# Kernel tuning notes

Measured on AMD Instinct MI355X. Metric: run time of the kernel, lower is better.

## Reference

```python
import jax, jax.numpy as jnp
import numpy as np
from jax import lax

# Module constants (from init_kwargs)
K = 1.0            # conductivity
H = 1.0 / 1023.0   # grid spacing
VALUE = 0.0        # Dirichlet boundary value
STENCIL = np.array([[0.0, 0.25, 0.0],
                    [0.25, 0.0, 0.25],
                    [0.0, 0.25, 0.0]], dtype=np.float32)


def setup_inputs() -> dict:
    key = jax.random.key(0)
    k1, k2 = jax.random.split(key)
    B, C, Hn, Wn = 16, 1, 1024, 1024
    u = jax.random.normal(k1, (B, C, Hn, Wn), dtype=jnp.float32)
    f = jax.random.normal(k2, (B, C, Hn, Wn), dtype=jnp.float32)
    # conv weight: (out=1, in=1, 3, 3), repeated over in_channels (=1 here)
    weight = jnp.asarray(STENCIL).reshape(1, 1, 3, 3)
    return {"u": u, "f": f, "weight": weight}


def reference(u, f, weight):
    # v = detached interior of u, padded with the Dirichlet value
    v_int = lax.stop_gradient(u[..., 1:-1, 1:-1])           # [B,1,H-2,W-2]
    v = jnp.pad(v_int, ((0, 0), (0, 0), (1, 1), (1, 1)),
                mode="constant", constant_values=VALUE)      # [B,1,H,W]
    # 5-point Jacobi stencil, VALID conv -> interior shape [B,1,H-2,W-2]
    conv = lax.conv_general_dilated(
        v, weight, window_strides=(1, 1), padding="VALID",
        dimension_numbers=("NCHW", "OIHW", "NCHW"))
    cof = -(H ** 2) / (K * 4.0)
    source = lax.stop_gradient((cof * f)[..., 1:-1, 1:-1])
    # interior <- stencil(v) + source; boundary stays at Dirichlet VALUE
    out = v.at[..., 1:-1, 1:-1].set(conv + source)
    return out
```

## Files before the change

### kernel.cpp

```cpp
#include <hip/hip_runtime.h>

#define IMG_W 1024
#define IMG_H 1024

typedef float v4f __attribute__((ext_vector_type(4)));

__global__ __launch_bounds__(256) void dir_rhs_kernel(
    const float* __restrict__ u,
    const float* __restrict__ f,
    const float* __restrict__ wt,
    float* __restrict__ out)
{
    const int orig = blockIdx.x;
    const int tile = (orig & 7) * 1024 + (orig >> 3);

    const int b    = tile >> 9;
    const int i0   = (tile & 511) << 1;
    const int tid  = threadIdx.x;
    const int wave = tid >> 6;
    const int lane = tid & 63;
    const int j0   = tid << 2;
    const size_t img = (size_t)b << 20;

    const float* ub = u + img;

    const bool le = (tid == 0);
    const bool re = (tid == 255);

    v4f c4[4]; float m[4];
    #pragma unroll
    for (int k = 0; k < 4; k++) {
        const int li = i0 - 1 + k;
        const int rc = li < 0 ? 0 : (li > IMG_H - 1 ? IMG_H - 1 : li);
        c4[k] = *(const v4f*)(ub + (size_t)rc * IMG_W + j0);
        m[k]  = (li >= 1 && li <= IMG_H - 2) ? 1.f : 0.f;
    }
    const float* fp = f + img + (size_t)i0 * IMG_W + j0;
    const v4f f0 = *(const v4f*)fp;
    const v4f f1 = *(const v4f*)(fp + IMG_W);

    const float w00 = wt[0], w01 = wt[1], w02 = wt[2];
    const float w10 = wt[3], w11 = wt[4], w12 = wt[5];
    const float w20 = wt[6], w21 = wt[7], w22 = wt[8];
    const float cof = (float)(-(1.0 / 1023.0) * (1.0 / 1023.0) / 4.0);

    #pragma unroll
    for (int k = 0; k < 4; k++) {
        c4[k] = c4[k] * m[k];
        if (le) c4[k].x = 0.f;
        if (re) c4[k].w = 0.f;
    }

    __shared__ float ledge[4][4];
    __shared__ float redge[4][4];
    if (lane == 0) {
        #pragma unroll
        for (int k = 0; k < 4; k++) ledge[wave][k] = c4[k].x;
    }
    if (lane == 63) {
        #pragma unroll
        for (int k = 0; k < 4; k++) redge[wave][k] = c4[k].w;
    }
    __syncthreads();

    float lh[4], rh[4];
    #pragma unroll
    for (int k = 0; k < 4; k++) {
        float l = __shfl_up(c4[k].w, 1);
        float r = __shfl_down(c4[k].x, 1);
        if (lane == 0)  l = (wave == 0) ? 0.f : redge[wave - 1][k];
        if (lane == 63) r = (wave == 3) ? 0.f : ledge[wave + 1][k];
        lh[k] = l; rh[k] = r;
    }

    const float keep0 = (i0 >= 1)         ? 1.f : 0.f;
    const float keep1 = (i0 <= IMG_H - 3) ? 1.f : 0.f;

    auto stencil = [&](int k, v4f fv, float keep) -> v4f {
        const v4f n = c4[k], cc = c4[k + 1], s = c4[k + 2];
        float r0 = cof * fv.x
                 + w00 * lh[k]     + w01 * n.x  + w02 * n.y
                 + w10 * lh[k + 1] + w11 * cc.x + w12 * cc.y
                 + w20 * lh[k + 2] + w21 * s.x  + w22 * s.y;
        float r1 = cof * fv.y
                 + w00 * n.x  + w01 * n.y  + w02 * n.z
                 + w10 * cc.x + w11 * cc.y + w12 * cc.z
                 + w20 * s.x  + w21 * s.y  + w22 * s.z;
        float r2 = cof * fv.z
                 + w00 * n.y  + w01 * n.z  + w02 * n.w
                 + w10 * cc.y + w11 * cc.z + w12 * cc.w
                 + w20 * s.y  + w21 * s.z  + w22 * s.w;
        float r3 = cof * fv.w
                 + w00 * n.z  + w01 * n.w  + w02 * rh[k]
                 + w10 * cc.z + w11 * cc.w + w12 * rh[k + 1]
                 + w20 * s.z  + w21 * s.w  + w22 * rh[k + 2];
        r0 *= keep; r1 *= keep; r2 *= keep; r3 *= keep;
        if (le) r0 = 0.f;
        if (re) r3 = 0.f;
        return (v4f){r0, r1, r2, r3};
    };

    const v4f o0 = stencil(0, f0, keep0);
    const v4f o1 = stencil(1, f1, keep1);

    float* ob = out + img + (size_t)i0 * IMG_W + j0;
    __builtin_nontemporal_store(o0, (v4f*)ob);
    __builtin_nontemporal_store(o1, (v4f*)(ob + IMG_W));
}

extern "C" void kernel_launch(void* const* d_in, const int* in_sizes, int n_in,
                              void* d_out, int out_size, void* d_ws, size_t ws_size,
                              hipStream_t stream) {
    const float* u  = (const float*)d_in[0];
    const float* f  = (const float*)d_in[1];
    const float* wt = (const float*)d_in[2];
    float* out = (float*)d_out;

    const int B = 16;
    dim3 grid(B * (IMG_H / 2));
    dim3 block(256);
    dir_rhs_kernel<<<grid, block, 0, stream>>>(u, f, wt, out);
}
```

Measured before the change: 176.2 us.

## Process eight rows per block with a rolling register window and prefetch

Each block now walks eight output rows in four steps of two. It keeps a sliding window of four u rows in registers, so the halo rows are not reloaded: u is read about 1.25x instead of 2x per output row. The next u and f rows are loaded before the current stencil is computed to overlap latency. f loads become nontemporal, and edge exchange uses double-buffered shared arrays with a barrier per step. This cuts the grid fourfold, which reduces parallelism and adds per-step synchronisation.

```diff
diff --git a/kernel.cpp b/kernel.cpp
--- a/kernel.cpp
+++ b/kernel.cpp
@@ -4,6 +4,10 @@
 #define IMG_H 1024
 
 typedef float v4f __attribute__((ext_vector_type(4)));
+
+__device__ __forceinline__ float rowmask(int li) {
+    return (li >= 1 && li <= IMG_H - 2) ? 1.f : 0.f;
+}
 
 __global__ __launch_bounds__(256) void dir_rhs_kernel(
     const float* __restrict__ u,
@@ -12,10 +16,10 @@
     float* __restrict__ out)
 {
     const int orig = blockIdx.x;
-    const int tile = (orig & 7) * 1024 + (orig >> 3);
+    const int tile = (orig & 7) * 256 + (orig >> 3);
 
-    const int b    = tile >> 9;
-    const int i0   = (tile & 511) << 1;
+    const int b    = tile >> 7;
+    const int g0   = (tile & 127) << 3;
     const int tid  = threadIdx.x;
     const int wave = tid >> 6;
     const int lane = tid & 63;
@@ -23,89 +27,135 @@
     const size_t img = (size_t)b << 20;
 
     const float* ub = u + img;
+    const float* fb = f + img;
 
     const bool le = (tid == 0);
     const bool re = (tid == 255);
-
-    v4f c4[4]; float m[4];
-    #pragma unroll
-    for (int k = 0; k < 4; k++) {
-        const int li = i0 - 1 + k;
-        const int rc = li < 0 ? 0 : (li > IMG_H - 1 ? IMG_H - 1 : li);
-        c4[k] = *(const v4f*)(ub + (size_t)rc * IMG_W + j0);
-        m[k]  = (li >= 1 && li <= IMG_H - 2) ? 1.f : 0.f;
-    }
-    const float* fp = f + img + (size_t)i0 * IMG_W + j0;
-    const v4f f0 = *(const v4f*)fp;
-    const v4f f1 = *(const v4f*)(fp + IMG_W);
 
     const float w00 = wt[0], w01 = wt[1], w02 = wt[2];
     const float w10 = wt[3], w11 = wt[4], w12 = wt[5];
     const float w20 = wt[6], w21 = wt[7], w22 = wt[8];
     const float cof = (float)(-(1.0 / 1023.0) * (1.0 / 1023.0) / 4.0);
 
+    __shared__ float ledge[2][4][4];
+    __shared__ float redge[2][4][4];
+
+    v4f cu[4];
+    float lh[4], rh[4];
+    {
+        v4f raw[4];
+        #pragma unroll
+        for (int k = 0; k < 4; k++) {
+            const int li = g0 - 1 + k;
+            const int rc = li < 0 ? 0 : (li > IMG_H - 1 ? IMG_H - 1 : li);
+            raw[k] = *(const v4f*)(ub + (size_t)rc * IMG_W + j0);
+        }
+        #pragma unroll
+        for (int k = 0; k < 4; k++) {
+            v4f t = raw[k] * rowmask(g0 - 1 + k);
+            if (le) t.x = 0.f;
+            if (re) t.w = 0.f;
+            cu[k] = t;
+        }
+        if (lane == 0) {
+            #pragma unroll
+            for (int k = 0; k < 4; k++) ledge[1][wave][k] = cu[k].x;
+        }
+        if (lane == 63) {
+            #pragma unroll
+            for (int k = 0; k < 4; k++) redge[1][wave][k] = cu[k].w;
+        }
+        __syncthreads();
+        #pragma unroll
+        for (int k = 0; k < 4; k++) {
+            float l = __shfl_up(cu[k].w, 1);
+            float r = __shfl_down(cu[k].x, 1);
+            if (lane == 0)  l = (wave == 0) ? 0.f : redge[1][wave - 1][k];
+            if (lane == 63) r = (wave == 3) ? 0.f : ledge[1][wave + 1][k];
+            lh[k] = l; rh[k] = r;
+        }
+    }
+    v4f fcur0 = __builtin_nontemporal_load((const v4f*)(fb + (size_t)g0 * IMG_W + j0));
+    v4f fcur1 = __builtin_nontemporal_load((const v4f*)(fb + (size_t)(g0 + 1) * IMG_W + j0));
+
     #pragma unroll
-    for (int k = 0; k < 4; k++) {
-        c4[k] = c4[k] * m[k];
-        if (le) c4[k].x = 0.f;
-        if (re) c4[k].w = 0.f;
+    for (int it = 0; it < 4; ++it) {
+        const int i0 = g0 + 2 * it;
+
+        v4f nu0, nu1, nf0, nf1;
+        if (it < 3) {
+            const int l3 = i0 + 3;
+            const int l4 = i0 + 4;
+            const int c3 = l3 > IMG_H - 1 ? IMG_H - 1 : l3;
+            const int c4 = l4 > IMG_H - 1 ? IMG_H - 1 : l4;
+            nu0 = *(const v4f*)(ub + (size_t)c3 * IMG_W + j0);
+            nu1 = *(const v4f*)(ub + (size_t)c4 * IMG_W + j0);
+            nf0 = __builtin_nontemporal_load((const v4f*)(fb + (size_t)(i0 + 2) * IMG_W + j0));
+            nf1 = __builtin_nontemporal_load((const v4f*)(fb + (size_t)(i0 + 3) * IMG_W + j0));
+        }
+
+        const float keep0 = (i0 >= 1 && i0 <= IMG_H - 2) ? 1.f : 0.f;
+        const float keep1 = (i0 + 1 <= IMG_H - 2) ? 1.f : 0.f;
+
+        auto stencil = [&](int k, v4f fv, float keep) -> v4f {
+            const v4f n = cu[k], cc = cu[k + 1], s = cu[k + 2];
+            float r0 = cof * fv.x
+                     + w00 * lh[k]     + w01 * n.x  + w02 * n.y
+                     + w10 * lh[k + 1] + w11 * cc.x + w12 * cc.y
+                     + w20 * lh[k + 2] + w21 * s.x  + w22 * s.y;
+            float r1 = cof * fv.y
+                     + w00 * n.x  + w01 * n.y  + w02 * n.z
+                     + w10 * cc.x + w11 * cc.y + w12 * cc.z
+                     + w20 * s.x  + w21 * s.y  + w22 * s.z;
+            float r2 = cof * fv.z
+                     + w00 * n.y  + w01 * n.z  + w02 * n.w
+                     + w10 * cc.y + w11 * cc.z + w12 * cc.w
+                     + w20 * s.y  + w21 * s.z  + w22 * s.w;
+            float r3 = cof * fv.w
+                     + w00 * n.z  + w01 * n.w  + w02 * rh[k]
+                     + w10 * cc.z + w11 * cc.w + w12 * rh[k + 1]
+                     + w20 * s.z  + w21 * s.w  + w22 * rh[k + 2];
+            r0 *= keep; r1 *= keep; r2 *= keep; r3 *= keep;
+            if (le) r0 = 0.f;
+            if (re) r3 = 0.f;
+            return (v4f){r0, r1, r2, r3};
+        };
+
+        const v4f o0 = stencil(0, fcur0, keep0);
+        const v4f o1 = stencil(1, fcur1, keep1);
+
+        float* ob = out + img + (size_t)i0 * IMG_W + j0;
+        __builtin_nontemporal_store(o0, (v4f*)ob);
+        __builtin_nontemporal_store(o1, (v4f*)(ob + IMG_W));
+
+        if (it < 3) {
+            const int p = it & 1;
+            v4f t3 = nu0 * rowmask(i0 + 3);
+            v4f t4 = nu1 * rowmask(i0 + 4);
+            if (le) { t3.x = 0.f; t4.x = 0.f; }
+            if (re) { t3.w = 0.f; t4.w = 0.f; }
+
+            if (lane == 0)  { ledge[p][wave][0] = t3.x; ledge[p][wave][1] = t4.x; }
+            if (lane == 63) { redge[p][wave][0] = t3.w; redge[p][wave][1] = t4.w; }
+            __syncthreads();
+
+            float l3 = __shfl_up(t3.w, 1),  r3 = __shfl_down(t3.x, 1);
+            float l4 = __shfl_up(t4.w, 1),  r4 = __shfl_down(t4.x, 1);
+            if (lane == 0) {
+                l3 = (wave == 0) ? 0.f : redge[p][wave - 1][0];
+                l4 = (wave == 0) ? 0.f : redge[p][wave - 1][1];
+            }
+            if (lane == 63) {
+                r3 = (wave == 3) ? 0.f : ledge[p][wave + 1][0];
+                r4 = (wave == 3) ? 0.f : ledge[p][wave + 1][1];
+            }
+
+            cu[0] = cu[2]; cu[1] = cu[3]; cu[2] = t3; cu[3] = t4;
+            lh[0] = lh[2]; lh[1] = lh[3]; lh[2] = l3; lh[3] = l4;
+            rh[0] = rh[2]; rh[1] = rh[3]; rh[2] = r3; rh[3] = r4;
+            fcur0 = nf0;   fcur1 = nf1;
+        }
     }
-
-    __shared__ float ledge[4][4];
-    __shared__ float redge[4][4];
-    if (lane == 0) {
-        #pragma unroll
-        for (int k = 0; k < 4; k++) ledge[wave][k] = c4[k].x;
-    }
-    if (lane == 63) {
-        #pragma unroll
-        for (int k = 0; k < 4; k++) redge[wave][k] = c4[k].w;
-    }
-    __syncthreads();
-
-    float lh[4], rh[4];
-    #pragma unroll
-    for (int k = 0; k < 4; k++) {
-        float l = __shfl_up(c4[k].w, 1);
-        float r = __shfl_down(c4[k].x, 1);
-        if (lane == 0)  l = (wave == 0) ? 0.f : redge[wave - 1][k];
-        if (lane == 63) r = (wave == 3) ? 0.f : ledge[wave + 1][k];
-        lh[k] = l; rh[k] = r;
-    }
-
-    const float keep0 = (i0 >= 1)         ? 1.f : 0.f;
-    const float keep1 = (i0 <= IMG_H - 3) ? 1.f : 0.f;
-
-    auto stencil = [&](int k, v4f fv, float keep) -> v4f {
-        const v4f n = c4[k], cc = c4[k + 1], s = c4[k + 2];
-        float r0 = cof * fv.x
-                 + w00 * lh[k]     + w01 * n.x  + w02 * n.y
-                 + w10 * lh[k + 1] + w11 * cc.x + w12 * cc.y
-                 + w20 * lh[k + 2] + w21 * s.x  + w22 * s.y;
-        float r1 = cof * fv.y
-                 + w00 * n.x  + w01 * n.y  + w02 * n.z
-                 + w10 * cc.x + w11 * cc.y + w12 * cc.z
-                 + w20 * s.x  + w21 * s.y  + w22 * s.z;
-        float r2 = cof * fv.z
-                 + w00 * n.y  + w01 * n.z  + w02 * n.w
-                 + w10 * cc.y + w11 * cc.z + w12 * cc.w
-                 + w20 * s.y  + w21 * s.z  + w22 * s.w;
-        float r3 = cof * fv.w
-                 + w00 * n.z  + w01 * n.w  + w02 * rh[k]
-                 + w10 * cc.z + w11 * cc.w + w12 * rh[k + 1]
-                 + w20 * s.z  + w21 * s.w  + w22 * rh[k + 2];
-        r0 *= keep; r1 *= keep; r2 *= keep; r3 *= keep;
-        if (le) r0 = 0.f;
-        if (re) r3 = 0.f;
-        return (v4f){r0, r1, r2, r3};
-    };
-
-    const v4f o0 = stencil(0, f0, keep0);
-    const v4f o1 = stencil(1, f1, keep1);
-
-    float* ob = out + img + (size_t)i0 * IMG_W + j0;
-    __builtin_nontemporal_store(o0, (v4f*)ob);
-    __builtin_nontemporal_store(o1, (v4f*)(ob + IMG_W));
 }
 
 extern "C" void kernel_launch(void* const* d_in, const int* in_sizes, int n_in,
@@ -117,7 +167,7 @@
     float* out = (float*)d_out;
 
     const int B = 16;
-    dim3 grid(B * (IMG_H / 2));
+    dim3 grid(B * (IMG_H / 8));
     dim3 block(256);
     dir_rhs_kernel<<<grid, block, 0, stream>>>(u, f, wt, out);
 }
```

Result: no change. 178.8 us (+1.5%).
